# Optimization experiments

Hardware: AMD Instinct MI355X
Metric: run time of the kernel (lower is better)

## Reference

```python
import jax, jax.numpy as jnp
import numpy as np

B, S, HID = 1, 2048, 2048
H, HD, DR = 16, 128, 64
CKV, CQ = 512, 1536
ROPE_BASE = 10000.0


def _rope_cos_sin(seq_len, dim, dtype):
    inv_freq = 1.0 / (ROPE_BASE ** (jnp.arange(0, dim, 2, dtype=jnp.float32) / dim))
    t = jnp.arange(seq_len, dtype=jnp.float32)
    freqs = jnp.outer(t, inv_freq)                      # [S, DR/2]
    emb = jnp.concatenate([freqs, freqs], axis=-1)      # [S, DR]
    return jnp.cos(emb).astype(dtype), jnp.sin(emb).astype(dtype)


def _rotate_half(x):
    x1, x2 = jnp.split(x, 2, axis=-1)
    return jnp.concatenate([-x2, x1], axis=-1)


def _xavier(key, fan_in, fan_out):
    lim = np.sqrt(6.0 / (fan_in + fan_out))
    return jax.random.uniform(key, (fan_in, fan_out), jnp.float32, -lim, lim)


def setup_inputs() -> dict:
    key = jax.random.key(0)
    ks = jax.random.split(key, 10)
    hidden_states = jax.random.normal(ks[0], (B, S, HID), jnp.float32)
    # causal mask: 1.0 where position is masked out (j > i)
    mask = jnp.triu(jnp.ones((S, S), jnp.float32), k=1)[None, None]  # [1,1,S,S]
    return {
        "hidden_states": hidden_states,
        "mask": mask,
        "W_DKV": _xavier(ks[1], HID, CKV),
        "W_UK": _xavier(ks[2], CKV, H * HD),
        "W_UV": _xavier(ks[3], CKV, H * HD),
        "W_DQ": _xavier(ks[4], HID, CQ),
        "W_UQ": _xavier(ks[5], CQ, H * HD),
        "W_QR": _xavier(ks[6], CQ, H * DR),
        "W_KR": _xavier(ks[7], HID, DR),
        "W_O": _xavier(ks[8], H * HD, HID),
    }


def reference(hidden_states, mask, W_DKV, W_UK, W_UV, W_DQ, W_UQ, W_QR, W_KR, W_O):
    b, s, _ = hidden_states.shape
    scale = 1.0 / np.sqrt(HD + DR)

    c_KV = hidden_states @ W_DKV                         # [B,S,CKV]
    k_C = (c_KV @ W_UK).reshape(b, s, H, HD)
    v = (c_KV @ W_UV).reshape(b, s, H, HD)
    c_Q = hidden_states @ W_DQ                           # [B,S,CQ]
    q_C = (c_Q @ W_UQ).reshape(b, s, H, HD)
    q_R = (c_Q @ W_QR).reshape(b, s, H, DR)
    k_R = (hidden_states @ W_KR).reshape(b, s, 1, DR)

    cos, sin = _rope_cos_sin(s, DR, hidden_states.dtype)
    cos = cos[None, :, None, :]                          # [1,S,1,DR]
    sin = sin[None, :, None, :]
    q_R = q_R * cos + _rotate_half(q_R) * sin
    k_R = k_R * cos + _rotate_half(k_R) * sin            # [B,S,1,DR], broadcast over heads

    q = jnp.concatenate([q_C, q_R], axis=-1)             # [B,S,H,HD+DR]
    k = jnp.concatenate([k_C, jnp.broadcast_to(k_R, (b, s, H, DR))], axis=-1)

    # [B,H,Sq,Sk]
    scores = jnp.einsum("bqhd,bkhd->bhqk", q, k) * scale
    if mask is not None:
        scores = scores + mask * -1e9                     # broadcast over heads
    probs = jax.nn.softmax(scores, axis=-1)
    out = jnp.einsum("bhqk,bkhd->bqhd", probs, v).reshape(b, s, H * HD)
    return out @ W_O
```

## Files before the change

### kernel.cpp

```cpp
#include <hip/hip_runtime.h>
#include <hip/hip_bf16.h>
#include <math.h>

typedef __hip_bfloat16 bf16;
typedef short s16x8 __attribute__((ext_vector_type(8)));
typedef unsigned short u16x8 __attribute__((ext_vector_type(8)));
typedef float f32x4 __attribute__((ext_vector_type(4)));

#define S_LEN 2048
#define NHEAD 16
#define HDIM  128
#define DROT  64

__device__ __forceinline__ float bf2f(unsigned short u) {
    union { unsigned int i; float f; } v;
    v.i = ((unsigned int)u) << 16;
    return v.f;
}
__device__ __forceinline__ unsigned short f2bf(float f) {
    union { float f; unsigned int i; } v;
    v.f = f;
    unsigned int r = (v.i + 0x7FFFu + ((v.i >> 16) & 1u)) >> 16;
    return (unsigned short)r;
}

__device__ __forceinline__ void load_lds16(const unsigned short* g, unsigned short* l) {
    __builtin_amdgcn_global_load_lds(
        (const __attribute__((address_space(1))) unsigned short*)g,
        (__attribute__((address_space(3))) unsigned short*)l, 16, 0, 0);
}

__device__ __forceinline__ bool is_bf16(const unsigned int* maskw) {
    return maskw[1] != 0x3F800000u;
}

struct PrepDesc {
    const void* in;
    unsigned short* out;
    int R, C, blk_start, nbx, kind;
};
struct PrepBatch { PrepDesc d[8]; };

__global__ __launch_bounds__(256)
void prep_kernel(PrepBatch b, const unsigned int* __restrict__ maskw) {
    const bool fb = is_bf16(maskw);
    __shared__ unsigned short t[64][80];
    PrepDesc dd = b.d[0];
    #pragma unroll
    for (int p = 1; p < 8; ++p)
        if ((int)blockIdx.x >= b.d[p].blk_start) dd = b.d[p];
    const int local = (int)blockIdx.x - dd.blk_start;
    const int tid = threadIdx.x;

    if (dd.kind == 1) {
        const size_t idx = ((size_t)local * 256 + tid) * 8;
        if (fb) {
            *(u16x8*)(dd.out + idx) = *(const u16x8*)((const unsigned short*)dd.in + idx);
        } else {
            const float* p = (const float*)dd.in + idx;
            float4 f0 = *(const float4*)p;
            float4 f1 = *(const float4*)(p + 4);
            u16x8 u;
            u[0] = f2bf(f0.x); u[1] = f2bf(f0.y); u[2] = f2bf(f0.z); u[3] = f2bf(f0.w);
            u[4] = f2bf(f1.x); u[5] = f2bf(f1.y); u[6] = f2bf(f1.z); u[7] = f2bf(f1.w);
            *(u16x8*)(dd.out + idx) = u;
        }
        return;
    }

    const int by = local / dd.nbx, bx = local - by * dd.nbx;
    const int r0 = by << 6, c0 = bx << 6;
    const int tr = tid >> 3;
    const int tc8 = (tid & 7) << 3;
    #pragma unroll
    for (int p = 0; p < 2; ++p) {
        const int r = tr + p * 32;
        const size_t off = (size_t)(r0 + r) * dd.C + c0 + tc8;
        unsigned short v[8];
        if (fb) {
            u16x8 u = *(const u16x8*)((const unsigned short*)dd.in + off);
            #pragma unroll
            for (int j = 0; j < 8; ++j) v[j] = u[j];
        } else {
            const float* p4 = (const float*)dd.in + off;
            float4 f0 = *(const float4*)p4;
            float4 f1 = *(const float4*)(p4 + 4);
            v[0] = f2bf(f0.x); v[1] = f2bf(f0.y); v[2] = f2bf(f0.z); v[3] = f2bf(f0.w);
            v[4] = f2bf(f1.x); v[5] = f2bf(f1.y); v[6] = f2bf(f1.z); v[7] = f2bf(f1.w);
        }
        #pragma unroll
        for (int j = 0; j < 8; ++j) t[tc8 + j][r] = v[j];
    }
    __syncthreads();
    #pragma unroll
    for (int p = 0; p < 2; ++p) {
        const int c = tr + p * 32;
        u16x8 u = *(const u16x8*)&t[c][tc8];
        *(u16x8*)(dd.out + (size_t)(c0 + c) * dd.R + r0 + tc8) = u;
    }
}

__global__ __launch_bounds__(256)
void transpose_conv(const void* __restrict__ in, unsigned short* __restrict__ out,
                    int R, int C, const unsigned int* __restrict__ maskw) {
    const bool fb = is_bf16(maskw);
    __shared__ unsigned short t[64][80];
    const int r0 = blockIdx.y << 6, c0 = blockIdx.x << 6;
    const int tid = threadIdx.x;
    const int tr = tid >> 3;
    const int tc8 = (tid & 7) << 3;
    #pragma unroll
    for (int p = 0; p < 2; ++p) {
        const int r = tr + p * 32;
        const size_t off = (size_t)(r0 + r) * C + c0 + tc8;
        unsigned short v[8];
        if (fb) {
            u16x8 u = *(const u16x8*)((const unsigned short*)in + off);
            #pragma unroll
            for (int j = 0; j < 8; ++j) v[j] = u[j];
        } else {
            const float* p4 = (const float*)in + off;
            float4 f0 = *(const float4*)p4;
            float4 f1 = *(const float4*)(p4 + 4);
            v[0] = f2bf(f0.x); v[1] = f2bf(f0.y); v[2] = f2bf(f0.z); v[3] = f2bf(f0.w);
            v[4] = f2bf(f1.x); v[5] = f2bf(f1.y); v[6] = f2bf(f1.z); v[7] = f2bf(f1.w);
        }
        #pragma unroll
        for (int j = 0; j < 8; ++j) t[tc8 + j][r] = v[j];
    }
    __syncthreads();
    #pragma unroll
    for (int p = 0; p < 2; ++p) {
        const int c = tr + p * 32;
        u16x8 u = *(const u16x8*)&t[c][tc8];
        *(u16x8*)(out + (size_t)(c0 + c) * R + r0 + tc8) = u;
    }
}

struct GemmDesc {
    const unsigned short* A;
    const unsigned short* Bt;
    void* C;
    int M, N, K;
    int nbx;
    int blk_start;
    int ct;
};
struct GemmBatch { GemmDesc d[4]; };

template <int NP, int CMODE>
__global__ __launch_bounds__(256)
void mfma_gemm2(GemmBatch batch, const unsigned int* __restrict__ maskw) {
    __shared__ __align__(16) unsigned short As[128 * 32];
    __shared__ __align__(16) unsigned short Bs[128 * 32];

    GemmDesc dd = batch.d[0];
    #pragma unroll
    for (int p = 1; p < NP; ++p)
        if ((int)blockIdx.x >= batch.d[p].blk_start) dd = batch.d[p];
    const int local = (int)blockIdx.x - dd.blk_start;
    const int by = local / dd.nbx;
    const int bx = local - by * dd.nbx;
    const int m0 = by << 7, n0 = bx << 7;
    const int K = dd.K;

    const int tid  = threadIdx.x;
    const int lane = tid & 63;
    const int w    = tid >> 6;
    const int wr = w >> 1, wc = w & 1;
    const int l15 = lane & 15, quad = lane >> 4, q8 = quad << 3;

    int srow[2], scol[2];
    #pragma unroll
    for (int i = 0; i < 2; ++i) {
        const int c = (2 * w + i) * 64 + lane;
        srow[i] = c >> 2;
        scol[i] = (c & 3) << 3;
    }

    f32x4 acc[4][4];
    #pragma unroll
    for (int i = 0; i < 4; ++i)
        #pragma unroll
        for (int j = 0; j < 4; ++j) {
            f32x4 z = {0.f, 0.f, 0.f, 0.f};
            acc[i][j] = z;
        }

    for (int k0 = 0; k0 < K; k0 += 32) {
        __syncthreads();
        #pragma unroll
        for (int i = 0; i < 2; ++i) {
            load_lds16(dd.A  + (size_t)(m0 + srow[i]) * K + k0 + scol[i],
                       As + (2 * w + i) * 512);
            load_lds16(dd.Bt + (size_t)(n0 + srow[i]) * K + k0 + scol[i],
                       Bs + (2 * w + i) * 512);
        }
        __syncthreads();
        s16x8 af[4], bf[4];
        #pragma unroll
        for (int mt = 0; mt < 4; ++mt)
            af[mt] = *(const s16x8*)&As[(wr * 64 + mt * 16 + l15) * 32 + q8];
        #pragma unroll
        for (int nt = 0; nt < 4; ++nt)
            bf[nt] = *(const s16x8*)&Bs[(wc * 64 + nt * 16 + l15) * 32 + q8];
        #pragma unroll
        for (int nt = 0; nt < 4; ++nt)
            #pragma unroll
            for (int mt = 0; mt < 4; ++mt)
                acc[mt][nt] = __builtin_amdgcn_mfma_f32_16x16x32_bf16(
                    af[mt], bf[nt], acc[mt][nt], 0, 0, 0);
    }

    bool cbf = true;
    if (CMODE == 2) cbf = is_bf16(maskw);
    const int M = dd.M, N = dd.N;
    #pragma unroll
    for (int mt = 0; mt < 4; ++mt)
        #pragma unroll
        for (int nt = 0; nt < 4; ++nt) {
            f32x4 d = acc[mt][nt];
            const int col  = n0 + wc * 64 + nt * 16 + l15;
            const int rowb = m0 + wr * 64 + mt * 16 + quad * 4;
            if (dd.ct) {
                ushort4 o;
                o.x = f2bf(d[0]); o.y = f2bf(d[1]); o.z = f2bf(d[2]); o.w = f2bf(d[3]);
                *(ushort4*)((unsigned short*)dd.C + (size_t)col * M + rowb) = o;
            } else if (cbf) {
                unsigned short* c = (unsigned short*)dd.C + (size_t)rowb * N + col;
                #pragma unroll
                for (int r = 0; r < 4; ++r) c[(size_t)r * N] = f2bf(d[r]);
            } else {
                float* c = (float*)dd.C + (size_t)rowb * N + col;
                #pragma unroll
                for (int r = 0; r < 4; ++r) c[(size_t)r * N] = d[r];
            }
        }
}

__global__ __launch_bounds__(256)
void rope_all(unsigned short* __restrict__ qR, unsigned short* __restrict__ kRb) {
    int bid = blockIdx.x;
    unsigned short* x;
    int nh, stride;
    if (bid < 4096) { x = qR; nh = 16; stride = 64; }
    else            { x = kRb; nh = 1; stride = 128; bid -= 4096; }
    const int idx = bid * 256 + threadIdx.x;
    const int d = idx & 31;
    const int rest = idx >> 5;
    const int h = rest % nh;
    const int s = rest / nh;
    if (s >= S_LEN) return;
    const float inv = powf(10000.0f, -(float)d * (1.0f / 32.0f));
    const float ang = (float)s * inv;
    float si, co;
    sincosf(ang, &si, &co);
    unsigned short* p = x + ((size_t)s * nh + h) * stride;
    const float x1 = bf2f(p[d]);
    const float x2 = bf2f(p[d + 32]);
    p[d]      = f2bf(x1 * co - x2 * si);
    p[d + 32] = f2bf(x2 * co + x1 * si);
}

__global__ __launch_bounds__(256)
void mfma_attn(const unsigned short* __restrict__ qC,
               const unsigned short* __restrict__ qR,
               const unsigned short* __restrict__ kC,
               const unsigned short* __restrict__ kRb,
               const unsigned short* __restrict__ vT,
               unsigned short* __restrict__ at) {
    __shared__ __align__(16) struct {
        unsigned short Ks[64][200];
        unsigned short Vs[128][72];
        unsigned short Ps[4][16][72];
    } sm;

    const int tid  = threadIdx.x;
    const int lane = tid & 63;
    const int w    = tid >> 6;
    const int l15 = lane & 15, quad = lane >> 4, q8 = quad << 3;
    const int h  = blockIdx.y;
    const int qb = (int)(gridDim.x - 1) - (int)blockIdx.x;
    const int q0 = qb << 6;
    const int qrow = q0 + w * 16 + l15;

    s16x8 qf[6];
    {
        const unsigned short* qCrow = qC + ((size_t)qrow * NHEAD + h) * HDIM;
        #pragma unroll
        for (int s = 0; s < 4; ++s)
            qf[s] = *(const s16x8*)(qCrow + s * 32 + q8);
        const unsigned short* qRrow = qR + ((size_t)qrow * NHEAD + h) * DROT;
        #pragma unroll
        for (int s = 0; s < 2; ++s)
            qf[4 + s] = *(const s16x8*)(qRrow + s * 32 + q8);
    }

    f32x4 accO[8];
    #pragma unroll
    for (int i = 0; i < 8; ++i) { f32x4 z = {0.f, 0.f, 0.f, 0.f}; accO[i] = z; }
    float slocal[4] = {0.f, 0.f, 0.f, 0.f};

    const float scale = 0.0721687836487032f;
    const int ntiles = (q0 >> 6) + 1;

    const int krow = tid >> 2, kcb = (tid & 3) * 48;
    const int vd = tid >> 1, vcb = (tid & 1) << 5;

    u16x8 kreg[6], vreg[4];
    {
        #pragma unroll
        for (int m = 0; m < 6; ++m) {
            const int c = kcb + m * 8;
            const unsigned short* src = (c < 128)
                ? kC + ((size_t)krow * NHEAD + h) * HDIM + c
                : kRb + (size_t)krow * 128 + (c - 128);
            kreg[m] = *(const u16x8*)src;
        }
        const unsigned short* vrow = vT + (size_t)(h * HDIM + vd) * S_LEN;
        #pragma unroll
        for (int m = 0; m < 4; ++m)
            vreg[m] = *(const u16x8*)(vrow + vcb + m * 8);
    }

    for (int t = 0; t < ntiles; ++t) {
        const int key0 = t << 6;
        __syncthreads();
        #pragma unroll
        for (int m = 0; m < 6; ++m)
            *(u16x8*)&sm.Ks[krow][kcb + m * 8] = kreg[m];
        #pragma unroll
        for (int m = 0; m < 4; ++m)
            *(u16x8*)&sm.Vs[vd][vcb + m * 8] = vreg[m];
        __syncthreads();

        if (t + 1 < ntiles) {
            const int kn = key0 + 64;
            #pragma unroll
            for (int m = 0; m < 6; ++m) {
                const int c = kcb + m * 8;
                const unsigned short* src = (c < 128)
                    ? kC + ((size_t)(kn + krow) * NHEAD + h) * HDIM + c
                    : kRb + (size_t)(kn + krow) * 128 + (c - 128);
                kreg[m] = *(const u16x8*)src;
            }
            const unsigned short* vrow = vT + (size_t)(h * HDIM + vd) * S_LEN + kn;
            #pragma unroll
            for (int m = 0; m < 4; ++m)
                vreg[m] = *(const u16x8*)(vrow + vcb + m * 8);
        }

        f32x4 sA[4];
        #pragma unroll
        for (int nt = 0; nt < 4; ++nt) { f32x4 z = {0.f, 0.f, 0.f, 0.f}; sA[nt] = z; }
        #pragma unroll
        for (int s = 0; s < 6; ++s)
            #pragma unroll
            for (int nt = 0; nt < 4; ++nt) {
                s16x8 kf = *(const s16x8*)&sm.Ks[nt * 16 + l15][s * 32 + q8];
                sA[nt] = __builtin_amdgcn_mfma_f32_16x16x32_bf16(qf[s], kf, sA[nt], 0, 0, 0);
            }

        const int rbase = q0 + w * 16 + quad * 4;
        const bool diag = (key0 + 63 > q0 + w * 16);
        float pv[4][4];
        #pragma unroll
        for (int nt = 0; nt < 4; ++nt) {
            const int col = key0 + nt * 16 + l15;
            #pragma unroll
            for (int r = 0; r < 4; ++r) {
                float s = sA[nt][r] * scale;
                if (diag && (col > rbase + r)) s = -1e30f;
                pv[nt][r] = __expf(s);
            }
        }
        #pragma unroll
        for (int r = 0; r < 4; ++r) {
            slocal[r] += (pv[0][r] + pv[1][r]) + (pv[2][r] + pv[3][r]);
            #pragma unroll
            for (int nt = 0; nt < 4; ++nt)
                sm.Ps[w][quad * 4 + r][nt * 16 + l15] = f2bf(pv[nt][r]);
        }

        s16x8 pf0 = *(const s16x8*)&sm.Ps[w][l15][q8];
        s16x8 pf1 = *(const s16x8*)&sm.Ps[w][l15][32 + q8];
        #pragma unroll
        for (int dt = 0; dt < 8; ++dt) {
            s16x8 vf0 = *(const s16x8*)&sm.Vs[dt * 16 + l15][q8];
            s16x8 vf1 = *(const s16x8*)&sm.Vs[dt * 16 + l15][32 + q8];
            accO[dt] = __builtin_amdgcn_mfma_f32_16x16x32_bf16(pf0, vf0, accO[dt], 0, 0, 0);
            accO[dt] = __builtin_amdgcn_mfma_f32_16x16x32_bf16(pf1, vf1, accO[dt], 0, 0, 0);
        }
    }

    float l_r[4];
    #pragma unroll
    for (int r = 0; r < 4; ++r) {
        float sum = slocal[r];
        #pragma unroll
        for (int off = 1; off < 16; off <<= 1)
            sum += __shfl_xor(sum, off, 64);
        l_r[r] = sum;
    }

    #pragma unroll
    for (int r = 0; r < 4; ++r) {
        const float linv = 1.f / l_r[r];
        const int row = q0 + w * 16 + quad * 4 + r;
        unsigned short* dst = at + (size_t)row * (NHEAD * HDIM) + h * HDIM + l15;
        #pragma unroll
        for (int dt = 0; dt < 8; ++dt)
            dst[dt * 16] = f2bf(accO[dt][r] * linv);
    }
}

extern "C" void kernel_launch(void* const* d_in, const int* in_sizes, int n_in,
                              void* d_out, int out_size, void* d_ws, size_t ws_size,
                              hipStream_t stream) {
    (void)in_sizes; (void)n_in; (void)out_size; (void)ws_size;

    const void* hs    = d_in[0];
    const unsigned int* maskw = (const unsigned int*)d_in[1];
    const void* W_DKV = d_in[2];
    const void* W_UK  = d_in[3];
    const void* W_UV  = d_in[4];
    const void* W_DQ  = d_in[5];
    const void* W_UQ  = d_in[6];
    const void* W_QR  = d_in[7];
    const void* W_KR  = d_in[8];
    const void* W_O   = d_in[9];

    const size_t M1 = 1048576;
    unsigned short* ws    = (unsigned short*)d_ws;
    unsigned short* cKV   = ws;
    unsigned short* cQ    = ws + 1 * M1;
    unsigned short* kC    = ws + 4 * M1;
    unsigned short* vT    = ws + 8 * M1;
    unsigned short* DKVt  = ws + 8 * M1;
    unsigned short* DQt   = ws + 9 * M1;
    unsigned short* qC    = ws + 12 * M1;
    unsigned short* hs_bf = ws + 12 * M1;
    unsigned short* qR    = ws + 16 * M1;
    unsigned short* kRb   = ws + 18 * M1;
    unsigned short* KRt   = ws + 18 * M1 + 262144;
    unsigned short* at    = ws + 18 * M1 + 524288;
    unsigned short* UKt   = at;
    unsigned short* UVt   = at + 1 * M1;
    unsigned short* QRt   = at + 2 * M1;
    unsigned short* UQt   = ws + 22 * M1 + 524288;
    unsigned short* WOt   = ws;

    const dim3 blk(256);

    {
        PrepBatch b{};
        b.d[0] = { hs,    hs_bf, 0, 0,           0,  0, 1 };
        b.d[1] = { W_DKV, DKVt,  2048,  512,  2048,  8, 0 };
        b.d[2] = { W_DQ,  DQt,   2048, 1536,  2304, 24, 0 };
        b.d[3] = { W_KR,  KRt,   2048,   64,  3072,  1, 0 };
        b.d[4] = { W_UK,  UKt,    512, 2048,  3104, 32, 0 };
        b.d[5] = { W_UV,  UVt,    512, 2048,  3360, 32, 0 };
        b.d[6] = { W_UQ,  UQt,   1536, 2048,  3616, 32, 0 };
        b.d[7] = { W_QR,  QRt,   1536, 1024,  4384, 16, 0 };
        prep_kernel<<<4768, blk, 0, stream>>>(b, maskw);
    }

    {
        GemmBatch b{};
        b.d[0] = { hs_bf, DQt,  (void*)cQ,  2048, 1536, 2048, 12,   0, 0 };
        b.d[1] = { hs_bf, DKVt, (void*)cKV, 2048,  512, 2048,  4, 192, 0 };
        b.d[2] = { hs_bf, KRt,  (void*)kRb, 2048,  128, 2048,  1, 256, 0 };
        b.d[3] = b.d[2];
        mfma_gemm2<3, 1><<<272, blk, 0, stream>>>(b, maskw);
    }

    {
        GemmBatch b{};
        b.d[0] = { cQ,  UQt, (void*)qC, 2048, 2048, 1536, 16,   0, 0 };
        b.d[1] = { cQ,  QRt, (void*)qR, 2048, 1024, 1536,  8, 256, 0 };
        b.d[2] = { cKV, UKt, (void*)kC, 2048, 2048,  512, 16, 384, 0 };
        b.d[3] = { cKV, UVt, (void*)vT, 2048, 2048,  512, 16, 640, 1 };
        mfma_gemm2<4, 1><<<896, blk, 0, stream>>>(b, maskw);
    }

    rope_all<<<4352, blk, 0, stream>>>(qR, kRb);

    transpose_conv<<<dim3(32, 32), blk, 0, stream>>>(W_O, WOt, 2048, 2048, maskw);

    mfma_attn<<<dim3(32, 16), blk, 0, stream>>>(qC, qR, kC, kRb, vT, at);

    {
        GemmBatch b{};
        b.d[0] = { at, WOt, d_out, 2048, 2048, 2048, 16, 0, 0 };
        b.d[1] = b.d[0]; b.d[2] = b.d[0]; b.d[3] = b.d[0];
        mfma_gemm2<1, 2><<<256, blk, 0, stream>>>(b, maskw);
    }
}
```

Measured before the change: 372.4 us.

## Fuse RoPE into GEMM epilogue, register-prefetch GEMM loads, double query rows per attention block

The GEMM now stages tiles through registers with a one-step software prefetch instead of direct global-to-LDS loads. It also applies the rotary embedding in the epilogue for the q_R and k_R projections, which removes the separate rope kernel and its extra bf16 round trip. The attention kernel processes 128 query rows per block (32 per wave) instead of 64, so each K/V tile loaded into shared memory is reused twice as much. In exchange, the attention grid has half as many blocks and each block uses more registers, which may reduce occupancy and load balance under the causal mask.

```diff
diff --git a/kernel.cpp b/kernel.cpp
--- a/kernel.cpp
+++ b/kernel.cpp
@@ -22,12 +22,6 @@
     v.f = f;
     unsigned int r = (v.i + 0x7FFFu + ((v.i >> 16) & 1u)) >> 16;
     return (unsigned short)r;
-}
-
-__device__ __forceinline__ void load_lds16(const unsigned short* g, unsigned short* l) {
-    __builtin_amdgcn_global_load_lds(
-        (const __attribute__((address_space(1))) unsigned short*)g,
-        (__attribute__((address_space(3))) unsigned short*)l, 16, 0, 0);
 }
 
 __device__ __forceinline__ bool is_bf16(const unsigned int* maskw) {
@@ -145,12 +139,13 @@
     int nbx;
     int blk_start;
     int ct;
+    int rope;
 };
 struct GemmBatch { GemmDesc d[4]; };
 
 template <int NP, int CMODE>
 __global__ __launch_bounds__(256)
-void mfma_gemm2(GemmBatch batch, const unsigned int* __restrict__ maskw) {
+void mfma_gemm3(GemmBatch batch, const unsigned int* __restrict__ maskw) {
     __shared__ __align__(16) unsigned short As[128 * 32];
     __shared__ __align__(16) unsigned short Bs[128 * 32];
 
@@ -170,13 +165,13 @@
     const int wr = w >> 1, wc = w & 1;
     const int l15 = lane & 15, quad = lane >> 4, q8 = quad << 3;
 
-    int srow[2], scol[2];
-    #pragma unroll
-    for (int i = 0; i < 2; ++i) {
-        const int c = (2 * w + i) * 64 + lane;
-        srow[i] = c >> 2;
-        scol[i] = (c & 3) << 3;
-    }
+    const int srow = tid & 127;
+    const int skof = (tid >> 7) << 4;
+    const unsigned short* Ap = dd.A  + (size_t)(m0 + srow) * K + skof;
+    const unsigned short* Bp = dd.Bt + (size_t)(n0 + srow) * K + skof;
+
+    u16x8 a0 = *(const u16x8*)Ap,       a1 = *(const u16x8*)(Ap + 8);
+    u16x8 b0 = *(const u16x8*)Bp,       b1 = *(const u16x8*)(Bp + 8);
 
     f32x4 acc[4][4];
     #pragma unroll
@@ -189,14 +184,17 @@
 
     for (int k0 = 0; k0 < K; k0 += 32) {
         __syncthreads();
-        #pragma unroll
-        for (int i = 0; i < 2; ++i) {
-            load_lds16(dd.A  + (size_t)(m0 + srow[i]) * K + k0 + scol[i],
-                       As + (2 * w + i) * 512);
-            load_lds16(dd.Bt + (size_t)(n0 + srow[i]) * K + k0 + scol[i],
-                       Bs + (2 * w + i) * 512);
-        }
+        *(u16x8*)&As[srow * 32 + skof]     = a0;
+        *(u16x8*)&As[srow * 32 + skof + 8] = a1;
+        *(u16x8*)&Bs[srow * 32 + skof]     = b0;
+        *(u16x8*)&Bs[srow * 32 + skof + 8] = b1;
         __syncthreads();
+        if (k0 + 32 < K) {
+            const unsigned short* An = Ap + k0 + 32;
+            const unsigned short* Bn = Bp + k0 + 32;
+            a0 = *(const u16x8*)An; a1 = *(const u16x8*)(An + 8);
+            b0 = *(const u16x8*)Bn; b1 = *(const u16x8*)(Bn + 8);
+        }
         s16x8 af[4], bf[4];
         #pragma unroll
         for (int mt = 0; mt < 4; ++mt)
@@ -210,6 +208,26 @@
             for (int mt = 0; mt < 4; ++mt)
                 acc[mt][nt] = __builtin_amdgcn_mfma_f32_16x16x32_bf16(
                     af[mt], bf[nt], acc[mt][nt], 0, 0, 0);
+    }
+
+    if (dd.rope) {
+        #pragma unroll
+        for (int nt = 0; nt < 2; ++nt) {
+            const float d = (float)(nt * 16 + l15);
+            const float inv = powf(10000.0f, -d * (1.0f / 32.0f));
+            #pragma unroll
+            for (int mt = 0; mt < 4; ++mt)
+                #pragma unroll
+                for (int r = 0; r < 4; ++r) {
+                    const int rowi = m0 + wr * 64 + mt * 16 + quad * 4 + r;
+                    float si, co;
+                    sincosf((float)rowi * inv, &si, &co);
+                    const float x1 = acc[mt][nt][r];
+                    const float x2 = acc[mt][nt + 2][r];
+                    acc[mt][nt][r]     = x1 * co - x2 * si;
+                    acc[mt][nt + 2][r] = x2 * co + x1 * si;
+                }
+        }
     }
 
     bool cbf = true;
@@ -239,30 +257,6 @@
 }
 
 __global__ __launch_bounds__(256)
-void rope_all(unsigned short* __restrict__ qR, unsigned short* __restrict__ kRb) {
-    int bid = blockIdx.x;
-    unsigned short* x;
-    int nh, stride;
-    if (bid < 4096) { x = qR; nh = 16; stride = 64; }
-    else            { x = kRb; nh = 1; stride = 128; bid -= 4096; }
-    const int idx = bid * 256 + threadIdx.x;
-    const int d = idx & 31;
-    const int rest = idx >> 5;
-    const int h = rest % nh;
-    const int s = rest / nh;
-    if (s >= S_LEN) return;
-    const float inv = powf(10000.0f, -(float)d * (1.0f / 32.0f));
-    const float ang = (float)s * inv;
-    float si, co;
-    sincosf(ang, &si, &co);
-    unsigned short* p = x + ((size_t)s * nh + h) * stride;
-    const float x1 = bf2f(p[d]);
-    const float x2 = bf2f(p[d + 32]);
-    p[d]      = f2bf(x1 * co - x2 * si);
-    p[d + 32] = f2bf(x2 * co + x1 * si);
-}
-
-__global__ __launch_bounds__(256)
 void mfma_attn(const unsigned short* __restrict__ qC,
                const unsigned short* __restrict__ qR,
                const unsigned short* __restrict__ kC,
@@ -272,7 +266,7 @@
     __shared__ __align__(16) struct {
         unsigned short Ks[64][200];
         unsigned short Vs[128][72];
-        unsigned short Ps[4][16][72];
+        unsigned short Ps[4][32][72];
     } sm;
 
     const int tid  = threadIdx.x;
@@ -280,29 +274,32 @@
     const int w    = tid >> 6;
     const int l15 = lane & 15, quad = lane >> 4, q8 = quad << 3;
     const int h  = blockIdx.y;
-    const int qb = (int)(gridDim.x - 1) - (int)blockIdx.x;
-    const int q0 = qb << 6;
-    const int qrow = q0 + w * 16 + l15;
-
-    s16x8 qf[6];
-    {
+    const int qb = 15 - (int)blockIdx.x;
+    const int q0 = qb << 7;
+
+    s16x8 qf[2][6];
+    #pragma unroll
+    for (int f = 0; f < 2; ++f) {
+        const int qrow = q0 + w * 32 + f * 16 + l15;
         const unsigned short* qCrow = qC + ((size_t)qrow * NHEAD + h) * HDIM;
         #pragma unroll
         for (int s = 0; s < 4; ++s)
-            qf[s] = *(const s16x8*)(qCrow + s * 32 + q8);
+            qf[f][s] = *(const s16x8*)(qCrow + s * 32 + q8);
         const unsigned short* qRrow = qR + ((size_t)qrow * NHEAD + h) * DROT;
         #pragma unroll
         for (int s = 0; s < 2; ++s)
-            qf[4 + s] = *(const s16x8*)(qRrow + s * 32 + q8);
-    }
-
-    f32x4 accO[8];
-    #pragma unroll
-    for (int i = 0; i < 8; ++i) { f32x4 z = {0.f, 0.f, 0.f, 0.f}; accO[i] = z; }
-    float slocal[4] = {0.f, 0.f, 0.f, 0.f};
+            qf[f][4 + s] = *(const s16x8*)(qRrow + s * 32 + q8);
+    }
+
+    f32x4 accO[2][8];
+    #pragma unroll
+    for (int f = 0; f < 2; ++f)
+        #pragma unroll
+        for (int i = 0; i < 8; ++i) { f32x4 z = {0.f, 0.f, 0.f, 0.f}; accO[f][i] = z; }
+    float slocal[2][4] = {{0.f}};
 
     const float scale = 0.0721687836487032f;
-    const int ntiles = (q0 >> 6) + 1;
+    const int ntiles = (q0 >> 6) + 2;
 
     const int krow = tid >> 2, kcb = (tid & 3) * 48;
     const int vd = tid >> 1, vcb = (tid & 1) << 5;
@@ -350,68 +347,79 @@
                 vreg[m] = *(const u16x8*)(vrow + vcb + m * 8);
         }
 
-        f32x4 sA[4];
-        #pragma unroll
-        for (int nt = 0; nt < 4; ++nt) { f32x4 z = {0.f, 0.f, 0.f, 0.f}; sA[nt] = z; }
+        f32x4 sA[2][4];
+        #pragma unroll
+        for (int f = 0; f < 2; ++f)
+            #pragma unroll
+            for (int nt = 0; nt < 4; ++nt) { f32x4 z = {0.f, 0.f, 0.f, 0.f}; sA[f][nt] = z; }
         #pragma unroll
         for (int s = 0; s < 6; ++s)
             #pragma unroll
             for (int nt = 0; nt < 4; ++nt) {
                 s16x8 kf = *(const s16x8*)&sm.Ks[nt * 16 + l15][s * 32 + q8];
-                sA[nt] = __builtin_amdgcn_mfma_f32_16x16x32_bf16(qf[s], kf, sA[nt], 0, 0, 0);
+                #pragma unroll
+                for (int f = 0; f < 2; ++f)
+                    sA[f][nt] = __builtin_amdgcn_mfma_f32_16x16x32_bf16(
+                        qf[f][s], kf, sA[f][nt], 0, 0, 0);
             }
 
-        const int rbase = q0 + w * 16 + quad * 4;
-        const bool diag = (key0 + 63 > q0 + w * 16);
-        float pv[4][4];
-        #pragma unroll
-        for (int nt = 0; nt < 4; ++nt) {
-            const int col = key0 + nt * 16 + l15;
+        #pragma unroll
+        for (int f = 0; f < 2; ++f) {
+            const int rb = q0 + w * 32 + f * 16;
+            const bool diag = (key0 + 63 > rb);
+            float pv[4][4];
+            #pragma unroll
+            for (int nt = 0; nt < 4; ++nt) {
+                const int col = key0 + nt * 16 + l15;
+                #pragma unroll
+                for (int r = 0; r < 4; ++r) {
+                    float s = sA[f][nt][r] * scale;
+                    if (diag && (col > rb + quad * 4 + r)) s = -1e30f;
+                    pv[nt][r] = __expf(s);
+                }
+            }
             #pragma unroll
             for (int r = 0; r < 4; ++r) {
-                float s = sA[nt][r] * scale;
-                if (diag && (col > rbase + r)) s = -1e30f;
-                pv[nt][r] = __expf(s);
+                slocal[f][r] += (pv[0][r] + pv[1][r]) + (pv[2][r] + pv[3][r]);
+                #pragma unroll
+                for (int nt = 0; nt < 4; ++nt)
+                    sm.Ps[w][f * 16 + quad * 4 + r][nt * 16 + l15] = f2bf(pv[nt][r]);
             }
         }
-        #pragma unroll
-        for (int r = 0; r < 4; ++r) {
-            slocal[r] += (pv[0][r] + pv[1][r]) + (pv[2][r] + pv[3][r]);
-            #pragma unroll
-            for (int nt = 0; nt < 4; ++nt)
-                sm.Ps[w][quad * 4 + r][nt * 16 + l15] = f2bf(pv[nt][r]);
-        }
-
-        s16x8 pf0 = *(const s16x8*)&sm.Ps[w][l15][q8];
-        s16x8 pf1 = *(const s16x8*)&sm.Ps[w][l15][32 + q8];
+
+        s16x8 pf[2][2];
+        #pragma unroll
+        for (int f = 0; f < 2; ++f) {
+            pf[f][0] = *(const s16x8*)&sm.Ps[w][f * 16 + l15][q8];
+            pf[f][1] = *(const s16x8*)&sm.Ps[w][f * 16 + l15][32 + q8];
+        }
         #pragma unroll
         for (int dt = 0; dt < 8; ++dt) {
             s16x8 vf0 = *(const s16x8*)&sm.Vs[dt * 16 + l15][q8];
             s16x8 vf1 = *(const s16x8*)&sm.Vs[dt * 16 + l15][32 + q8];
-            accO[dt] = __builtin_amdgcn_mfma_f32_16x16x32_bf16(pf0, vf0, accO[dt], 0, 0, 0);
-            accO[dt] = __builtin_amdgcn_mfma_f32_16x16x32_bf16(pf1, vf1, accO[dt], 0, 0, 0);
-        }
-    }
-
-    float l_r[4];
-    #pragma unroll
-    for (int r = 0; r < 4; ++r) {
-        float sum = slocal[r];
-        #pragma unroll
-        for (int off = 1; off < 16; off <<= 1)
-            sum += __shfl_xor(sum, off, 64);
-        l_r[r] = sum;
-    }
-
-    #pragma unroll
-    for (int r = 0; r < 4; ++r) {
-        const float linv = 1.f / l_r[r];
-        const int row = q0 + w * 16 + quad * 4 + r;
-        unsigned short* dst = at + (size_t)row * (NHEAD * HDIM) + h * HDIM + l15;
-        #pragma unroll
-        for (int dt = 0; dt < 8; ++dt)
-            dst[dt * 16] = f2bf(accO[dt][r] * linv);
-    }
+            #pragma unroll
+            for (int f = 0; f < 2; ++f) {
+                accO[f][dt] = __builtin_amdgcn_mfma_f32_16x16x32_bf16(pf[f][0], vf0, accO[f][dt], 0, 0, 0);
+                accO[f][dt] = __builtin_amdgcn_mfma_f32_16x16x32_bf16(pf[f][1], vf1, accO[f][dt], 0, 0, 0);
+            }
+        }
+    }
+
+    #pragma unroll
+    for (int f = 0; f < 2; ++f)
+        #pragma unroll
+        for (int r = 0; r < 4; ++r) {
+            float sum = slocal[f][r];
+            #pragma unroll
+            for (int off = 1; off < 16; off <<= 1)
+                sum += __shfl_xor(sum, off, 64);
+            const float linv = 1.f / sum;
+            const int row = q0 + w * 32 + f * 16 + quad * 4 + r;
+            unsigned short* dst = at + (size_t)row * (NHEAD * HDIM) + h * HDIM + l15;
+            #pragma unroll
+            for (int dt = 0; dt < 8; ++dt)
+                dst[dt * 16] = f2bf(accO[f][dt][r] * linv);
+        }
 }
 
 extern "C" void kernel_launch(void* const* d_in, const int* in_sizes, int n_in,
@@ -467,32 +475,30 @@
 
     {
         GemmBatch b{};
-        b.d[0] = { hs_bf, DQt,  (void*)cQ,  2048, 1536, 2048, 12,   0, 0 };
-        b.d[1] = { hs_bf, DKVt, (void*)cKV, 2048,  512, 2048,  4, 192, 0 };
-        b.d[2] = { hs_bf, KRt,  (void*)kRb, 2048,  128, 2048,  1, 256, 0 };
+        b.d[0] = { hs_bf, DQt,  (void*)cQ,  2048, 1536, 2048, 12,   0, 0, 0 };
+        b.d[1] = { hs_bf, DKVt, (void*)cKV, 2048,  512, 2048,  4, 192, 0, 0 };
+        b.d[2] = { hs_bf, KRt,  (void*)kRb, 2048,  128, 2048,  1, 256, 0, 1 };
         b.d[3] = b.d[2];
-        mfma_gemm2<3, 1><<<272, blk, 0, stream>>>(b, maskw);
+        mfma_gemm3<3, 1><<<272, blk, 0, stream>>>(b, maskw);
     }
 
     {
         GemmBatch b{};
-        b.d[0] = { cQ,  UQt, (void*)qC, 2048, 2048, 1536, 16,   0, 0 };
-        b.d[1] = { cQ,  QRt, (void*)qR, 2048, 1024, 1536,  8, 256, 0 };
-        b.d[2] = { cKV, UKt, (void*)kC, 2048, 2048,  512, 16, 384, 0 };
-        b.d[3] = { cKV, UVt, (void*)vT, 2048, 2048,  512, 16, 640, 1 };
-        mfma_gemm2<4, 1><<<896, blk, 0, stream>>>(b, maskw);
-    }
-
-    rope_all<<<4352, blk, 0, stream>>>(qR, kRb);
+        b.d[0] = { cQ,  UQt, (void*)qC, 2048, 2048, 1536, 16,   0, 0, 0 };
+        b.d[1] = { cQ,  QRt, (void*)qR, 2048, 1024, 1536,  8, 256, 0, 1 };
+        b.d[2] = { cKV, UKt, (void*)kC, 2048, 2048,  512, 16, 384, 0, 0 };
+        b.d[3] = { cKV, UVt, (void*)vT, 2048, 2048,  512, 16, 640, 1, 0 };
+        mfma_gemm3<4, 1><<<896, blk, 0, stream>>>(b, maskw);
+    }
 
     transpose_conv<<<dim3(32, 32), blk, 0, stream>>>(W_O, WOt, 2048, 2048, maskw);
 
-    mfma_attn<<<dim3(32, 16), blk, 0, stream>>>(qC, qR, kC, kRb, vT, at);
+    mfma_attn<<<dim3(16, 16), blk, 0, stream>>>(qC, qR, kC, kRb, vT, at);
 
     {
         GemmBatch b{};
-        b.d[0] = { at, WOt, d_out, 2048, 2048, 2048, 16, 0, 0 };
+        b.d[0] = { at, WOt, d_out, 2048, 2048, 2048, 16, 0, 0, 0 };
         b.d[1] = b.d[0]; b.d[2] = b.d[0]; b.d[3] = b.d[0];
-        mfma_gemm2<1, 2><<<256, blk, 0, stream>>>(b, maskw);
-    }
-}
+        mfma_gemm3<1, 2><<<256, blk, 0, stream>>>(b, maskw);
+    }
+}
```

New measurement: 496.9 us. 1.33x slower.
